# Optimization experiments

Hardware: AMD Instinct MI355X
Metric: run time of the kernel (lower is better)

The kernel has to match this reference:

```python
import jax, jax.numpy as jnp
import numpy as np

B, N, E, D = 1024, 6, 6, 1280  # batch, n_node, n_edge_types, state_dim
N_STEPS = 5
EDGES = [[1, 1, 2], [1, 2, 3], [1, 3, 4], [2, 4, 3], [2, 5, 4], [3, 6, 4]]


def make_adjacency():
    a = np.zeros([N, N * E * 2], dtype=np.float32)
    for src, et, tgt in EDGES:
        a[tgt - 1, (et - 1) * N + src - 1] = 1.0
        a[src - 1, (et - 1 + E) * N + tgt - 1] = 1.0
    return jnp.asarray(a)


def setup_inputs() -> dict:
    key = jax.random.key(0)
    ks = jax.random.split(key, 8)
    std = 0.02  # matches m.weight.data.normal_(0.0, 0.02)
    return {
        "x": jax.random.normal(ks[0], (B, N, D), jnp.float32),
        "A": make_adjacency(),  # [N, 2*E*N] structural 0/1 adjacency
        "W_in": std * jax.random.normal(ks[1], (E, D, D), jnp.float32),
        "b_in": jnp.zeros((E, D), jnp.float32),
        "W_out": std * jax.random.normal(ks[2], (E, D, D), jnp.float32),
        "b_out": jnp.zeros((E, D), jnp.float32),
        "W_r": std * jax.random.normal(ks[3], (3 * D, D), jnp.float32),
        "b_r": jnp.zeros((D,), jnp.float32),
        "W_z": std * jax.random.normal(ks[4], (3 * D, D), jnp.float32),
        "b_z": jnp.zeros((D,), jnp.float32),
        "W_t": std * jax.random.normal(ks[5], (3 * D, D), jnp.float32),
        "b_t": jnp.zeros((D,), jnp.float32),
    }


def reference(x, A, W_in, b_in, W_out, b_out, W_r, b_r, W_z, b_z, W_t, b_t):
    # x: [B, N, D] pooled per-part features (post backbone avgpool+transpose).
    A_in = A[:, : N * E]   # [N, E*N]
    A_out = A[:, N * E:]   # [N, E*N]
    gx = x
    for _ in range(N_STEPS):
        # per-edge-type linears; edge-type-major layout matches torch view(-1, N*E, D)
        in_s = jnp.einsum("bnd,edf->benf", gx, W_in) + b_in[:, None, :]   # [B,E,N,D]
        out_s = jnp.einsum("bnd,edf->benf", gx, W_out) + b_out[:, None, :]
        in_s = in_s.reshape(gx.shape[0], E * N, D)
        out_s = out_s.reshape(gx.shape[0], E * N, D)
        a_in = jnp.einsum("nm,bmd->bnd", A_in, in_s)     # bmm with adjacency
        a_out = jnp.einsum("nm,bmd->bnd", A_out, out_s)
        a = jnp.concatenate([a_in, a_out, gx], axis=-1)  # [B,N,3D]
        r = jax.nn.sigmoid(a @ W_r + b_r)
        z = jax.nn.sigmoid(a @ W_z + b_z)
        joined = jnp.concatenate([a_in, a_out, r * gx], axis=-1)
        h_hat = jnp.tanh(joined @ W_t + b_t)
        gx = (1.0 - z) * gx + z * h_hat
    # transpose(1,2) then flatten(1): [B, D, N] -> [B, D*N]
    return jnp.transpose(gx, (0, 2, 1)).reshape(gx.shape[0], D * N)
```

## Files before the change

kernel.cpp:

```cpp
#include <hip/hip_runtime.h>
#include <hip/hip_bf16.h>
#include <stdint.h>

#define D 1280
#define ND 6
#define BATCH 1024
#define ROWSTRIDE (ND*D)
#define WELEM (D*D)
#define WIOF(e) ((e)*WELEM)
#define WOOF(e) ((6+(e))*WELEM)
#define WROF (12*WELEM)
#define WZOF (15*WELEM)
#define WTOF (18*WELEM)
#define WTOT (21*WELEM)
#define ABUF (BATCH*ROWSTRIDE)
#define AINO (ABUF)
#define AOUTO (2*ABUF)
#define RGO (3*ABUF)
#define S3D (3*D)

typedef unsigned int u32;
typedef unsigned short u16;
typedef __bf16 bf16x8 __attribute__((ext_vector_type(8)));
typedef float f32x4 __attribute__((ext_vector_type(4)));

struct Term { int a_off; int b_off; int b_stride; int bias_off; };
struct Job  { int nterms; int epi; int node; int flag; Term t[3]; };

__constant__ Job JOBS[28] = {
  {1,0,1,0, {{0*D, WIOF(0), D, 0*D},{0,0,0,0},{0,0,0,0}}},
  {2,0,2,0, {{0*D, WIOF(1), D, 1*D},{1*D, WIOF(3), D, 3*D},{0,0,0,0}}},
  {3,0,3,0, {{0*D, WIOF(2), D, 2*D},{1*D, WIOF(4), D, 4*D},{2*D, WIOF(5), D, 5*D}}},
  {3,0,0,1, {{1*D, WOOF(0), D, 0*D},{2*D, WOOF(1), D, 1*D},{3*D, WOOF(2), D, 2*D}}},
  {2,0,1,1, {{2*D, WOOF(3), D, 3*D},{3*D, WOOF(4), D, 4*D},{0,0,0,0}}},
  {1,0,2,1, {{3*D, WOOF(5), D, 5*D},{0,0,0,0},{0,0,0,0}}},
  {2,1,0,0, {{AOUTO+0*D, WROF+1*D, S3D, 0},{0*D, WROF+2*D, S3D, 0},{0,0,0,0}}},
  {3,1,1,0, {{AINO+1*D, WROF+0*D, S3D, 0},{AOUTO+1*D, WROF+1*D, S3D, 0},{1*D, WROF+2*D, S3D, 0}}},
  {3,1,2,0, {{AINO+2*D, WROF+0*D, S3D, 0},{AOUTO+2*D, WROF+1*D, S3D, 0},{2*D, WROF+2*D, S3D, 0}}},
  {2,1,3,0, {{AINO+3*D, WROF+0*D, S3D, 0},{3*D, WROF+2*D, S3D, 0},{0,0,0,0}}},
  {1,1,4,0, {{4*D, WROF+2*D, S3D, 0},{0,0,0,0},{0,0,0,0}}},
  {1,1,5,0, {{5*D, WROF+2*D, S3D, 0},{0,0,0,0},{0,0,0,0}}},
  {2,2,0,0, {{AOUTO+0*D, WZOF+1*D, S3D, 0},{0*D, WZOF+2*D, S3D, 0},{0,0,0,0}}},
  {3,2,1,0, {{AINO+1*D, WZOF+0*D, S3D, 0},{AOUTO+1*D, WZOF+1*D, S3D, 0},{1*D, WZOF+2*D, S3D, 0}}},
  {3,2,2,0, {{AINO+2*D, WZOF+0*D, S3D, 0},{AOUTO+2*D, WZOF+1*D, S3D, 0},{2*D, WZOF+2*D, S3D, 0}}},
  {2,2,3,0, {{AINO+3*D, WZOF+0*D, S3D, 0},{3*D, WZOF+2*D, S3D, 0},{0,0,0,0}}},
  {1,2,4,0, {{4*D, WZOF+2*D, S3D, 0},{0,0,0,0},{0,0,0,0}}},
  {1,2,5,0, {{5*D, WZOF+2*D, S3D, 0},{0,0,0,0},{0,0,0,0}}},
  {1,3,0,0, {{AOUTO+0*D, WTOF+1*D, S3D, 0},{0,0,0,0},{0,0,0,0}}},
  {2,3,1,0, {{AINO+1*D, WTOF+0*D, S3D, 0},{AOUTO+1*D, WTOF+1*D, S3D, 0},{0,0,0,0}}},
  {2,3,2,0, {{AINO+2*D, WTOF+0*D, S3D, 0},{AOUTO+2*D, WTOF+1*D, S3D, 0},{0,0,0,0}}},
  {1,3,3,0, {{AINO+3*D, WTOF+0*D, S3D, 0},{0,0,0,0},{0,0,0,0}}},
  {1,4,0,1, {{RGO+0*D, WTOF+2*D, S3D, 0},{0,0,0,0},{0,0,0,0}}},
  {1,4,1,1, {{RGO+1*D, WTOF+2*D, S3D, 0},{0,0,0,0},{0,0,0,0}}},
  {1,4,2,1, {{RGO+2*D, WTOF+2*D, S3D, 0},{0,0,0,0},{0,0,0,0}}},
  {1,4,3,1, {{RGO+3*D, WTOF+2*D, S3D, 0},{0,0,0,0},{0,0,0,0}}},
  {1,4,4,0, {{RGO+4*D, WTOF+2*D, S3D, 0},{0,0,0,0},{0,0,0,0}}},
  {1,4,5,0, {{RGO+5*D, WTOF+2*D, S3D, 0},{0,0,0,0},{0,0,0,0}}},
};

__device__ __forceinline__ void gload16(const void* g, void* l) {
  __builtin_amdgcn_global_load_lds((const __attribute__((address_space(1))) u32*)g,
                                   (__attribute__((address_space(3))) u32*)l, 16, 0, 0);
}
__device__ __forceinline__ float sig_(float x){ return 1.f/(1.f+__expf(-x)); }
__device__ __forceinline__ float tanh_(float x){ float e=__expf(2.f*x); return 1.f-2.f/(e+1.f); }

__device__ __forceinline__ u16 f2b(float f){ __hip_bfloat16 v = __float2bfloat16(f); return *(u16*)&v; }

__global__ __launch_bounds__(256)
void gemm_batched(u16* act, const u16* __restrict__ wb,
                  float* __restrict__ gx, float* __restrict__ zbuf, float* __restrict__ tp,
                  const float* __restrict__ b_in, const float* __restrict__ b_out,
                  const float* __restrict__ b_r, const float* __restrict__ b_z,
                  const float* __restrict__ b_t, int job_base) {
  const int bid = blockIdx.x;
  const Job jb = JOBS[job_base + bid/80];
  const int t80 = bid % 80;
  const int m0 = (t80/10)*128;
  const int n0 = (t80%10)*128;
  const int tid = threadIdx.x;
  const int lane = tid & 63;
  const int w = tid >> 6;
  const int wm = ((w>>1)<<6);
  const int wn = ((w&1)<<6);

  __shared__ __align__(16) u16 lsA[128*64];
  __shared__ __align__(16) u16 lsB[128*64];

  f32x4 acc[4][4];
#pragma unroll
  for (int i=0;i<4;i++)
#pragma unroll
    for (int j=0;j<4;j++) acc[i][j] = (f32x4)(0.0f);

  const int srow = lane>>3;
  const int scol = (lane&7)*8;

  for (int term=0; term<jb.nterms; ++term) {
    const u16* Ab = act + jb.t[term].a_off;
    const u16* Bb = wb  + jb.t[term].b_off;
    const int bstr = jb.t[term].b_stride;
    for (int kt=0; kt<20; ++kt) {
      const int kk = kt*64;
#pragma unroll
      for (int i=0;i<4;i++) {
        const int rr = w*32 + i*8 + srow;
        gload16(Ab + (size_t)(m0+rr)*ROWSTRIDE + kk + scol, &lsA[(w*32+i*8)*64]);
        gload16(Bb + (size_t)(n0+rr)*bstr      + kk + scol, &lsB[(w*32+i*8)*64]);
      }
      __syncthreads();
#pragma unroll
      for (int ks=0; ks<2; ++ks) {
        bf16x8 af[4], bfr[4];
#pragma unroll
        for (int i=0;i<4;i++) {
          af[i]  = *(const bf16x8*)&lsA[(wm + i*16 + (lane&15))*64 + ks*32 + (lane>>4)*8];
          bfr[i] = *(const bf16x8*)&lsB[(wn + i*16 + (lane&15))*64 + ks*32 + (lane>>4)*8];
        }
#pragma unroll
        for (int i=0;i<4;i++)
#pragma unroll
          for (int j=0;j<4;j++)
            acc[i][j] = __builtin_amdgcn_mfma_f32_16x16x32_bf16(af[i], bfr[j], acc[i][j], 0,0,0);
      }
      __syncthreads();
    }
  }

  const int r0 = m0 + wm + ((lane>>4)<<2);
  const int c0 = n0 + wn + (lane&15);
  const int node = jb.node;

  if (jb.epi == 0) {
    const float* bias = jb.flag ? b_out : b_in;
    u16* outp = act + (jb.flag ? AOUTO : AINO) + node*D;
    float bsum[4];
#pragma unroll
    for (int j=0;j<4;j++) {
      float s = 0.f;
      for (int t2=0;t2<jb.nterms;t2++) s += bias[jb.t[t2].bias_off + c0 + j*16];
      bsum[j] = s;
    }
#pragma unroll
    for (int i=0;i<4;i++)
#pragma unroll
      for (int j=0;j<4;j++)
#pragma unroll
        for (int r=0;r<4;r++) {
          int row = r0 + i*16 + r, col = c0 + j*16;
          outp[(size_t)row*ROWSTRIDE + col] = f2b(acc[i][j][r] + bsum[j]);
        }
  } else if (jb.epi == 1) {
#pragma unroll
    for (int i=0;i<4;i++)
#pragma unroll
      for (int j=0;j<4;j++)
#pragma unroll
        for (int r=0;r<4;r++) {
          int row = r0 + i*16 + r, col = c0 + j*16;
          size_t idx = (size_t)row*ROWSTRIDE + node*D + col;
          float rr = sig_(acc[i][j][r] + b_r[col]);
          act[RGO + idx] = f2b(rr * gx[idx]);
        }
  } else if (jb.epi == 2) {
#pragma unroll
    for (int i=0;i<4;i++)
#pragma unroll
      for (int j=0;j<4;j++)
#pragma unroll
        for (int r=0;r<4;r++) {
          int row = r0 + i*16 + r, col = c0 + j*16;
          size_t idx = (size_t)row*ROWSTRIDE + node*D + col;
          zbuf[idx] = sig_(acc[i][j][r] + b_z[col]);
        }
  } else if (jb.epi == 3) {
#pragma unroll
    for (int i=0;i<4;i++)
#pragma unroll
      for (int j=0;j<4;j++)
#pragma unroll
        for (int r=0;r<4;r++) {
          int row = r0 + i*16 + r, col = c0 + j*16;
          size_t idx = (size_t)row*ROWSTRIDE + node*D + col;
          tp[idx] = acc[i][j][r];
        }
  } else {
#pragma unroll
    for (int i=0;i<4;i++)
#pragma unroll
      for (int j=0;j<4;j++)
#pragma unroll
        for (int r=0;r<4;r++) {
          int row = r0 + i*16 + r, col = c0 + j*16;
          size_t idx = (size_t)row*ROWSTRIDE + node*D + col;
          float tv = acc[i][j][r] + b_t[col] + (jb.flag ? tp[idx] : 0.f);
          float h = tanh_(tv);
          float zv = zbuf[idx];
          float g = gx[idx];
          float ng = (1.f - zv)*g + zv*h;
          gx[idx] = ng;
          act[idx] = f2b(ng);
        }
  }
}

__global__ void conv_weights(const float* __restrict__ wi, const float* __restrict__ wo,
                             const float* __restrict__ wr, const float* __restrict__ wz,
                             const float* __restrict__ wt, u16* __restrict__ wb) {
  int bid = blockIdx.x;
  int base = 0; int j = 0;
  for (; j < 15; ++j) {
    int R_ = (j < 12) ? 1280 : 3840;
    int tiles = (R_/32)*40;
    if (bid < base + tiles) break;
    base += tiles;
  }
  const int R = (j < 12) ? 1280 : 3840;
  const int C = 1280;
  const float* src; int doff;
  if (j < 6)        { src = wi + (size_t)j*WELEM;     doff = WIOF(j); }
  else if (j < 12)  { src = wo + (size_t)(j-6)*WELEM; doff = WOOF(j-6); }
  else if (j == 12) { src = wr;                       doff = WROF; }
  else if (j == 13) { src = wz;                       doff = WZOF; }
  else              { src = wt;                       doff = WTOF; }
  int tt = bid - base;
  int tr = tt / 40, tc = tt % 40;
  __shared__ float tile[32][33];
  int tx = threadIdx.x, ty = threadIdx.y;
#pragma unroll
  for (int k=0;k<4;k++)
    tile[ty+8*k][tx] = src[(size_t)(tr*32+ty+8*k)*C + tc*32+tx];
  __syncthreads();
  u16* dst = wb + doff;
#pragma unroll
  for (int k=0;k<4;k++)
    dst[(size_t)(tc*32+ty+8*k)*R + tr*32+tx] = f2b(tile[tx][ty+8*k]);
}

__global__ void init_gx(const float* __restrict__ x, float* __restrict__ gx, u16* __restrict__ gxb) {
  for (size_t i = (size_t)blockIdx.x*blockDim.x + threadIdx.x; i < (size_t)ABUF;
       i += (size_t)gridDim.x*blockDim.x) {
    float v = x[i];
    gx[i] = v;
    gxb[i] = f2b(v);
  }
}

__global__ void final_out(const float* __restrict__ gx, float* __restrict__ out) {
  int b = blockIdx.x;
  const float* g = gx + (size_t)b*ROWSTRIDE;
  float* o = out + (size_t)b*ROWSTRIDE;
  for (int jj = threadIdx.x; jj < ROWSTRIDE; jj += blockDim.x) {
    int n = jj % ND, d = jj / ND;
    o[jj] = g[n*D + d];
  }
}

extern "C" void kernel_launch(void* const* d_in, const int* in_sizes, int n_in,
                              void* d_out, int out_size, void* d_ws, size_t ws_size,
                              hipStream_t stream) {
  (void)in_sizes; (void)n_in; (void)out_size; (void)ws_size;
  const float* x  = (const float*)d_in[0];
  const float* Wi = (const float*)d_in[2];
  const float* bi = (const float*)d_in[3];
  const float* Wo = (const float*)d_in[4];
  const float* bo = (const float*)d_in[5];
  const float* Wr = (const float*)d_in[6];
  const float* br = (const float*)d_in[7];
  const float* Wz = (const float*)d_in[8];
  const float* bz = (const float*)d_in[9];
  const float* Wt = (const float*)d_in[10];
  const float* bt = (const float*)d_in[11];
  float* out = (float*)d_out;

  u16* wb  = (u16*)d_ws;
  u16* act = wb + WTOT;
  float* gx = (float*)(act + (size_t)4*ABUF);
  float* zb = gx + ABUF;
  float* tp = zb + ABUF;

  conv_weights<<<33600, dim3(32,8,1), 0, stream>>>(Wi, Wo, Wr, Wz, Wt, wb);
  init_gx<<<2048, 256, 0, stream>>>(x, gx, act);
  for (int s = 0; s < 5; ++s) {
    gemm_batched<<<480, 256, 0, stream>>>(act, wb, gx, zb, tp, bi, bo, br, bz, bt, 0);
    gemm_batched<<<1280,256, 0, stream>>>(act, wb, gx, zb, tp, bi, bo, br, bz, bt, 6);
    gemm_batched<<<480, 256, 0, stream>>>(act, wb, gx, zb, tp, bi, bo, br, bz, bt, 22);
  }
  final_out<<<BATCH, 256, 0, stream>>>(gx, out);
}
```

Measured before the change: 1.909 ms.

## Rewrite GEMM with 256x256 tiles, LDS double buffering, and split edge-term combine

Replaces the 128x128 single-buffered GEMM with a 512-thread, 256x256-tile kernel. It double-buffers LDS through async global-to-LDS loads, uses an XOR-swizzled LDS layout, raises instruction priority around the MFMA blocks, and interleaves loads of the next tile with compute in four phases. The multi-term edge GEMMs are split into 12 single-term jobs whose bf16 partial results land in a scratch buffer. A new combine kernel then sums those partials, which adds an extra launch and an extra round trip to memory. The gate jobs are reordered so the heavier ones are scheduled first.

```diff
diff --git a/kernel.cpp b/kernel.cpp
--- a/kernel.cpp
+++ b/kernel.cpp
@@ -18,37 +18,45 @@
 #define AOUTO (2*ABUF)
 #define RGO (3*ABUF)
 #define S3D (3*D)
+#define SLICE (BATCH*D)
 
 typedef unsigned int u32;
 typedef unsigned short u16;
 typedef __bf16 bf16x8 __attribute__((ext_vector_type(8)));
 typedef float f32x4 __attribute__((ext_vector_type(4)));
+typedef u16 u16x8 __attribute__((ext_vector_type(8)));
 
 struct Term { int a_off; int b_off; int b_stride; int bias_off; };
 struct Job  { int nterms; int epi; int node; int flag; Term t[3]; };
 
-__constant__ Job JOBS[28] = {
-  {1,0,1,0, {{0*D, WIOF(0), D, 0*D},{0,0,0,0},{0,0,0,0}}},
-  {2,0,2,0, {{0*D, WIOF(1), D, 1*D},{1*D, WIOF(3), D, 3*D},{0,0,0,0}}},
-  {3,0,3,0, {{0*D, WIOF(2), D, 2*D},{1*D, WIOF(4), D, 4*D},{2*D, WIOF(5), D, 5*D}}},
-  {3,0,0,1, {{1*D, WOOF(0), D, 0*D},{2*D, WOOF(1), D, 1*D},{3*D, WOOF(2), D, 2*D}}},
-  {2,0,1,1, {{2*D, WOOF(3), D, 3*D},{3*D, WOOF(4), D, 4*D},{0,0,0,0}}},
-  {1,0,2,1, {{3*D, WOOF(5), D, 5*D},{0,0,0,0},{0,0,0,0}}},
-  {2,1,0,0, {{AOUTO+0*D, WROF+1*D, S3D, 0},{0*D, WROF+2*D, S3D, 0},{0,0,0,0}}},
+__constant__ Job JOBS[34] = {
+  {1,0,0, 0, {{0*D, WIOF(0), D, 0*D},{0,0,0,0},{0,0,0,0}}},
+  {1,0,1, 0, {{0*D, WIOF(1), D, 1*D},{0,0,0,0},{0,0,0,0}}},
+  {1,0,2, 0, {{0*D, WIOF(2), D, 2*D},{0,0,0,0},{0,0,0,0}}},
+  {1,0,3, 0, {{1*D, WIOF(3), D, 3*D},{0,0,0,0},{0,0,0,0}}},
+  {1,0,4, 0, {{1*D, WIOF(4), D, 4*D},{0,0,0,0},{0,0,0,0}}},
+  {1,0,5, 0, {{2*D, WIOF(5), D, 5*D},{0,0,0,0},{0,0,0,0}}},
+  {1,0,6, 1, {{1*D, WOOF(0), D, 0*D},{0,0,0,0},{0,0,0,0}}},
+  {1,0,7, 1, {{2*D, WOOF(1), D, 1*D},{0,0,0,0},{0,0,0,0}}},
+  {1,0,8, 1, {{3*D, WOOF(2), D, 2*D},{0,0,0,0},{0,0,0,0}}},
+  {1,0,9, 1, {{2*D, WOOF(3), D, 3*D},{0,0,0,0},{0,0,0,0}}},
+  {1,0,10,1, {{3*D, WOOF(4), D, 4*D},{0,0,0,0},{0,0,0,0}}},
+  {1,0,11,1, {{3*D, WOOF(5), D, 5*D},{0,0,0,0},{0,0,0,0}}},
   {3,1,1,0, {{AINO+1*D, WROF+0*D, S3D, 0},{AOUTO+1*D, WROF+1*D, S3D, 0},{1*D, WROF+2*D, S3D, 0}}},
   {3,1,2,0, {{AINO+2*D, WROF+0*D, S3D, 0},{AOUTO+2*D, WROF+1*D, S3D, 0},{2*D, WROF+2*D, S3D, 0}}},
+  {3,2,1,0, {{AINO+1*D, WZOF+0*D, S3D, 0},{AOUTO+1*D, WZOF+1*D, S3D, 0},{1*D, WZOF+2*D, S3D, 0}}},
+  {3,2,2,0, {{AINO+2*D, WZOF+0*D, S3D, 0},{AOUTO+2*D, WZOF+1*D, S3D, 0},{2*D, WZOF+2*D, S3D, 0}}},
+  {2,1,0,0, {{AOUTO+0*D, WROF+1*D, S3D, 0},{0*D, WROF+2*D, S3D, 0},{0,0,0,0}}},
   {2,1,3,0, {{AINO+3*D, WROF+0*D, S3D, 0},{3*D, WROF+2*D, S3D, 0},{0,0,0,0}}},
+  {2,2,0,0, {{AOUTO+0*D, WZOF+1*D, S3D, 0},{0*D, WZOF+2*D, S3D, 0},{0,0,0,0}}},
+  {2,2,3,0, {{AINO+3*D, WZOF+0*D, S3D, 0},{3*D, WZOF+2*D, S3D, 0},{0,0,0,0}}},
+  {2,3,1,0, {{AINO+1*D, WTOF+0*D, S3D, 0},{AOUTO+1*D, WTOF+1*D, S3D, 0},{0,0,0,0}}},
+  {2,3,2,0, {{AINO+2*D, WTOF+0*D, S3D, 0},{AOUTO+2*D, WTOF+1*D, S3D, 0},{0,0,0,0}}},
   {1,1,4,0, {{4*D, WROF+2*D, S3D, 0},{0,0,0,0},{0,0,0,0}}},
   {1,1,5,0, {{5*D, WROF+2*D, S3D, 0},{0,0,0,0},{0,0,0,0}}},
-  {2,2,0,0, {{AOUTO+0*D, WZOF+1*D, S3D, 0},{0*D, WZOF+2*D, S3D, 0},{0,0,0,0}}},
-  {3,2,1,0, {{AINO+1*D, WZOF+0*D, S3D, 0},{AOUTO+1*D, WZOF+1*D, S3D, 0},{1*D, WZOF+2*D, S3D, 0}}},
-  {3,2,2,0, {{AINO+2*D, WZOF+0*D, S3D, 0},{AOUTO+2*D, WZOF+1*D, S3D, 0},{2*D, WZOF+2*D, S3D, 0}}},
-  {2,2,3,0, {{AINO+3*D, WZOF+0*D, S3D, 0},{3*D, WZOF+2*D, S3D, 0},{0,0,0,0}}},
   {1,2,4,0, {{4*D, WZOF+2*D, S3D, 0},{0,0,0,0},{0,0,0,0}}},
   {1,2,5,0, {{5*D, WZOF+2*D, S3D, 0},{0,0,0,0},{0,0,0,0}}},
   {1,3,0,0, {{AOUTO+0*D, WTOF+1*D, S3D, 0},{0,0,0,0},{0,0,0,0}}},
-  {2,3,1,0, {{AINO+1*D, WTOF+0*D, S3D, 0},{AOUTO+1*D, WTOF+1*D, S3D, 0},{0,0,0,0}}},
-  {2,3,2,0, {{AINO+2*D, WTOF+0*D, S3D, 0},{AOUTO+2*D, WTOF+1*D, S3D, 0},{0,0,0,0}}},
   {1,3,3,0, {{AINO+3*D, WTOF+0*D, S3D, 0},{0,0,0,0},{0,0,0,0}}},
   {1,4,0,1, {{RGO+0*D, WTOF+2*D, S3D, 0},{0,0,0,0},{0,0,0,0}}},
   {1,4,1,1, {{RGO+1*D, WTOF+2*D, S3D, 0},{0,0,0,0},{0,0,0,0}}},
@@ -58,150 +66,282 @@
   {1,4,5,0, {{RGO+5*D, WTOF+2*D, S3D, 0},{0,0,0,0},{0,0,0,0}}},
 };
 
+struct Cmb { int dst; int np; int p[3]; };
+__constant__ Cmb CMBS[6] = {
+  {AINO + 1*D, 1, {0,0,0}},
+  {AINO + 2*D, 2, {1,3,0}},
+  {AINO + 3*D, 3, {2,4,5}},
+  {AOUTO+ 0*D, 3, {6,7,8}},
+  {AOUTO+ 1*D, 2, {9,10,0}},
+  {AOUTO+ 2*D, 1, {11,0,0}},
+};
+
 __device__ __forceinline__ void gload16(const void* g, void* l) {
   __builtin_amdgcn_global_load_lds((const __attribute__((address_space(1))) u32*)g,
                                    (__attribute__((address_space(3))) u32*)l, 16, 0, 0);
 }
 __device__ __forceinline__ float sig_(float x){ return 1.f/(1.f+__expf(-x)); }
 __device__ __forceinline__ float tanh_(float x){ float e=__expf(2.f*x); return 1.f-2.f/(e+1.f); }
-
 __device__ __forceinline__ u16 f2b(float f){ __hip_bfloat16 v = __float2bfloat16(f); return *(u16*)&v; }
-
-__global__ __launch_bounds__(256)
-void gemm_batched(u16* act, const u16* __restrict__ wb,
-                  float* __restrict__ gx, float* __restrict__ zbuf, float* __restrict__ tp,
-                  const float* __restrict__ b_in, const float* __restrict__ b_out,
-                  const float* __restrict__ b_r, const float* __restrict__ b_z,
-                  const float* __restrict__ b_t, int job_base) {
-  const int bid = blockIdx.x;
-  const Job jb = JOBS[job_base + bid/80];
-  const int t80 = bid % 80;
-  const int m0 = (t80/10)*128;
-  const int n0 = (t80%10)*128;
-  const int tid = threadIdx.x;
+__device__ __forceinline__ float b2f(u16 v){ return __uint_as_float(((u32)v)<<16); }
+
+__device__ __forceinline__ void bar() {
+  asm volatile("" ::: "memory");
+  __builtin_amdgcn_s_barrier();
+  asm volatile("" ::: "memory");
+}
+#define VMCNT(n) asm volatile("s_waitcnt vmcnt(" #n ")" ::: "memory")
+
+__device__ __forceinline__ void stage_part(int jidx, const u16* __restrict__ act,
+    const u16* __restrict__ wb, u16* ls, int m0, int n0, int Ts, int part,
+    int lane, int w) {
+  const int tm = (Ts >= 40) ? 2 : (Ts >= 20 ? 1 : 0);
+  const int kt = Ts - tm*20;
+  const Term& t = JOBS[jidx].t[tm];
+  const u16* G; int gstr; int row0;
+  if (part < 2) { G = act + t.a_off; gstr = ROWSTRIDE;  row0 = m0 + part*128; }
+  else          { G = wb  + t.b_off; gstr = t.b_stride; row0 = n0 + (part-2)*128; }
+  u16* lbase = ls + (part < 2 ? 0 : 32768) + (((Ts&1)*2 + (part&1))*8192);
+  const u16* gk = G + kt*64;
+#pragma unroll
+  for (int l = 0; l < 2; ++l) {
+    const int rb = l*64 + w*8;
+    const int r  = rb + (lane>>3);
+    const int c  = ((lane&7)*8) ^ ((r&4) ? 16 : 0);
+    gload16(gk + (size_t)(row0 + r)*gstr + c, lbase + rb*64);
+  }
+}
+
+__global__ __launch_bounds__(512, 1)
+void gemm256(u16* __restrict__ act, const u16* __restrict__ wb, u16* __restrict__ part,
+             float* __restrict__ gx, float* __restrict__ zbuf, float* __restrict__ tp,
+             const float* __restrict__ b_in, const float* __restrict__ b_out,
+             const float* __restrict__ b_r, const float* __restrict__ b_z,
+             const float* __restrict__ b_t, int job_base) {
+  extern __shared__ u16 ls[];
+  const int bid  = blockIdx.x;
+  const int jidx = job_base + bid/20;
+  const int tile = bid%20;
+  const int m0 = (tile/5)*256;
+  const int n0 = (tile%5)*256;
+  const int tid  = threadIdx.x;
   const int lane = tid & 63;
-  const int w = tid >> 6;
-  const int wm = ((w>>1)<<6);
-  const int wn = ((w&1)<<6);
-
-  __shared__ __align__(16) u16 lsA[128*64];
-  __shared__ __align__(16) u16 lsB[128*64];
-
-  f32x4 acc[4][4];
-#pragma unroll
-  for (int i=0;i<4;i++)
-#pragma unroll
-    for (int j=0;j<4;j++) acc[i][j] = (f32x4)(0.0f);
-
-  const int srow = lane>>3;
-  const int scol = (lane&7)*8;
-
-  for (int term=0; term<jb.nterms; ++term) {
-    const u16* Ab = act + jb.t[term].a_off;
-    const u16* Bb = wb  + jb.t[term].b_off;
-    const int bstr = jb.t[term].b_stride;
-    for (int kt=0; kt<20; ++kt) {
-      const int kk = kt*64;
-#pragma unroll
-      for (int i=0;i<4;i++) {
-        const int rr = w*32 + i*8 + srow;
-        gload16(Ab + (size_t)(m0+rr)*ROWSTRIDE + kk + scol, &lsA[(w*32+i*8)*64]);
-        gload16(Bb + (size_t)(n0+rr)*bstr      + kk + scol, &lsB[(w*32+i*8)*64]);
+  const int w    = tid >> 6;
+  const int wm   = w >> 2;
+  const int wn   = w & 3;
+  const int NT   = JOBS[jidx].nterms * 20;
+
+  f32x4 acc[8][4];
+#pragma unroll
+  for (int f=0; f<8; ++f)
+#pragma unroll
+    for (int g=0; g<4; ++g) acc[f][g] = (f32x4)(0.0f);
+
+  stage_part(jidx, act, wb, ls, m0, n0, 0, 0, lane, w);
+  stage_part(jidx, act, wb, ls, m0, n0, 0, 1, lane, w);
+  stage_part(jidx, act, wb, ls, m0, n0, 0, 2, lane, w);
+  stage_part(jidx, act, wb, ls, m0, n0, 0, 3, lane, w);
+  stage_part(jidx, act, wb, ls, m0, n0, 1, 2, lane, w);
+  stage_part(jidx, act, wb, ls, m0, n0, 1, 3, lane, w);
+  VMCNT(4);
+  bar();
+
+  const int lr = lane & 15;
+  const int lc = (lane >> 4) * 8;
+
+  for (int T = 0; T < NT; ++T) {
+    const int d = T & 1;
+    const u16* Ah = ls + (d*2 + wm)*8192;
+    const u16* Bh = ls + 32768 + (d*2 + (wn>>1))*8192;
+    bf16x8 af[4][2], b01[2][2], b23[2][2];
+
+#pragma unroll
+    for (int fi=0; fi<4; ++fi)
+#pragma unroll
+      for (int ks=0; ks<2; ++ks) {
+        const int r = fi*16 + lr;
+        const int c = (ks*32 + lc) ^ ((r&4) ? 16 : 0);
+        af[fi][ks] = *(const bf16x8*)(Ah + r*64 + c);
       }
-      __syncthreads();
+#pragma unroll
+    for (int g=0; g<2; ++g)
 #pragma unroll
       for (int ks=0; ks<2; ++ks) {
-        bf16x8 af[4], bfr[4];
-#pragma unroll
-        for (int i=0;i<4;i++) {
-          af[i]  = *(const bf16x8*)&lsA[(wm + i*16 + (lane&15))*64 + ks*32 + (lane>>4)*8];
-          bfr[i] = *(const bf16x8*)&lsB[(wn + i*16 + (lane&15))*64 + ks*32 + (lane>>4)*8];
+        const int r = (wn&1)*64 + g*16 + lr;
+        const int c = (ks*32 + lc) ^ ((r&4) ? 16 : 0);
+        b01[g][ks] = *(const bf16x8*)(Bh + r*64 + c);
+      }
+    if (T+1 < NT) stage_part(jidx, act, wb, ls, m0, n0, T+1, 0, lane, w);
+    bar();
+    __builtin_amdgcn_s_setprio(1);
+#pragma unroll
+    for (int fi=0; fi<4; ++fi)
+#pragma unroll
+      for (int g=0; g<2; ++g)
+#pragma unroll
+        for (int ks=0; ks<2; ++ks)
+          acc[fi][g] = __builtin_amdgcn_mfma_f32_16x16x32_bf16(af[fi][ks], b01[g][ks], acc[fi][g], 0,0,0);
+    __builtin_amdgcn_s_setprio(0);
+    bar();
+
+#pragma unroll
+    for (int g=0; g<2; ++g)
+#pragma unroll
+      for (int ks=0; ks<2; ++ks) {
+        const int r = (wn&1)*64 + (g+2)*16 + lr;
+        const int c = (ks*32 + lc) ^ ((r&4) ? 16 : 0);
+        b23[g][ks] = *(const bf16x8*)(Bh + r*64 + c);
+      }
+    if (T+1 < NT) stage_part(jidx, act, wb, ls, m0, n0, T+1, 1, lane, w);
+    bar();
+    __builtin_amdgcn_s_setprio(1);
+#pragma unroll
+    for (int fi=0; fi<4; ++fi)
+#pragma unroll
+      for (int g=0; g<2; ++g)
+#pragma unroll
+        for (int ks=0; ks<2; ++ks)
+          acc[fi][g+2] = __builtin_amdgcn_mfma_f32_16x16x32_bf16(af[fi][ks], b23[g][ks], acc[fi][g+2], 0,0,0);
+    __builtin_amdgcn_s_setprio(0);
+    bar();
+
+#pragma unroll
+    for (int fi=0; fi<4; ++fi)
+#pragma unroll
+      for (int ks=0; ks<2; ++ks) {
+        const int r = (fi+4)*16 + lr;
+        const int c = (ks*32 + lc) ^ ((r&4) ? 16 : 0);
+        af[fi][ks] = *(const bf16x8*)(Ah + r*64 + c);
+      }
+    if (T+2 < NT) stage_part(jidx, act, wb, ls, m0, n0, T+2, 2, lane, w);
+    bar();
+    __builtin_amdgcn_s_setprio(1);
+#pragma unroll
+    for (int fi=0; fi<4; ++fi)
+#pragma unroll
+      for (int g=0; g<2; ++g)
+#pragma unroll
+        for (int ks=0; ks<2; ++ks)
+          acc[fi+4][g] = __builtin_amdgcn_mfma_f32_16x16x32_bf16(af[fi][ks], b01[g][ks], acc[fi+4][g], 0,0,0);
+    __builtin_amdgcn_s_setprio(0);
+    bar();
+
+    if (T+2 < NT) {
+      stage_part(jidx, act, wb, ls, m0, n0, T+2, 3, lane, w);
+      VMCNT(4);
+    } else {
+      VMCNT(0);
+    }
+    bar();
+    __builtin_amdgcn_s_setprio(1);
+#pragma unroll
+    for (int fi=0; fi<4; ++fi)
+#pragma unroll
+      for (int g=0; g<2; ++g)
+#pragma unroll
+        for (int ks=0; ks<2; ++ks)
+          acc[fi+4][g+2] = __builtin_amdgcn_mfma_f32_16x16x32_bf16(af[fi][ks], b23[g][ks], acc[fi+4][g+2], 0,0,0);
+    __builtin_amdgcn_s_setprio(0);
+    bar();
+  }
+
+  const int epi  = JOBS[jidx].epi;
+  const int node = JOBS[jidx].node;
+  const int flag = JOBS[jidx].flag;
+  const int r0 = m0 + wm*128 + ((lane>>4)<<2);
+  const int c0 = n0 + wn*64 + (lane&15);
+
+  if (epi == 0) {
+    const float* bias = (flag ? b_out : b_in) + JOBS[jidx].t[0].bias_off;
+    u16* outp = part + (size_t)node*SLICE;
+#pragma unroll
+    for (int g=0; g<4; ++g) {
+      const int col = c0 + g*16;
+      const float bv = bias[col];
+#pragma unroll
+      for (int f=0; f<8; ++f)
+#pragma unroll
+        for (int r=0; r<4; ++r)
+          outp[(size_t)(r0 + f*16 + r)*D + col] = f2b(acc[f][g][r] + bv);
+    }
+  } else if (epi == 1) {
+#pragma unroll
+    for (int g=0; g<4; ++g) {
+      const int col = c0 + g*16;
+      const float bv = b_r[col];
+#pragma unroll
+      for (int f=0; f<8; ++f)
+#pragma unroll
+        for (int r=0; r<4; ++r) {
+          const size_t idx = (size_t)(r0 + f*16 + r)*ROWSTRIDE + node*D + col;
+          act[RGO + idx] = f2b(sig_(acc[f][g][r] + bv) * gx[idx]);
         }
-#pragma unroll
-        for (int i=0;i<4;i++)
-#pragma unroll
-          for (int j=0;j<4;j++)
-            acc[i][j] = __builtin_amdgcn_mfma_f32_16x16x32_bf16(af[i], bfr[j], acc[i][j], 0,0,0);
-      }
-      __syncthreads();
-    }
-  }
-
-  const int r0 = m0 + wm + ((lane>>4)<<2);
-  const int c0 = n0 + wn + (lane&15);
-  const int node = jb.node;
-
-  if (jb.epi == 0) {
-    const float* bias = jb.flag ? b_out : b_in;
-    u16* outp = act + (jb.flag ? AOUTO : AINO) + node*D;
-    float bsum[4];
-#pragma unroll
-    for (int j=0;j<4;j++) {
-      float s = 0.f;
-      for (int t2=0;t2<jb.nterms;t2++) s += bias[jb.t[t2].bias_off + c0 + j*16];
-      bsum[j] = s;
-    }
-#pragma unroll
-    for (int i=0;i<4;i++)
-#pragma unroll
-      for (int j=0;j<4;j++)
-#pragma unroll
-        for (int r=0;r<4;r++) {
-          int row = r0 + i*16 + r, col = c0 + j*16;
-          outp[(size_t)row*ROWSTRIDE + col] = f2b(acc[i][j][r] + bsum[j]);
+    }
+  } else if (epi == 2) {
+#pragma unroll
+    for (int g=0; g<4; ++g) {
+      const int col = c0 + g*16;
+      const float bv = b_z[col];
+#pragma unroll
+      for (int f=0; f<8; ++f)
+#pragma unroll
+        for (int r=0; r<4; ++r) {
+          const size_t idx = (size_t)(r0 + f*16 + r)*ROWSTRIDE + node*D + col;
+          zbuf[idx] = sig_(acc[f][g][r] + bv);
         }
-  } else if (jb.epi == 1) {
-#pragma unroll
-    for (int i=0;i<4;i++)
-#pragma unroll
-      for (int j=0;j<4;j++)
-#pragma unroll
-        for (int r=0;r<4;r++) {
-          int row = r0 + i*16 + r, col = c0 + j*16;
-          size_t idx = (size_t)row*ROWSTRIDE + node*D + col;
-          float rr = sig_(acc[i][j][r] + b_r[col]);
-          act[RGO + idx] = f2b(rr * gx[idx]);
+    }
+  } else if (epi == 3) {
+#pragma unroll
+    for (int g=0; g<4; ++g) {
+      const int col = c0 + g*16;
+#pragma unroll
+      for (int f=0; f<8; ++f)
+#pragma unroll
+        for (int r=0; r<4; ++r) {
+          const size_t idx = (size_t)(r0 + f*16 + r)*ROWSTRIDE + node*D + col;
+          tp[idx] = acc[f][g][r];
         }
-  } else if (jb.epi == 2) {
-#pragma unroll
-    for (int i=0;i<4;i++)
-#pragma unroll
-      for (int j=0;j<4;j++)
-#pragma unroll
-        for (int r=0;r<4;r++) {
-          int row = r0 + i*16 + r, col = c0 + j*16;
-          size_t idx = (size_t)row*ROWSTRIDE + node*D + col;
-          zbuf[idx] = sig_(acc[i][j][r] + b_z[col]);
-        }
-  } else if (jb.epi == 3) {
-#pragma unroll
-    for (int i=0;i<4;i++)
-#pragma unroll
-      for (int j=0;j<4;j++)
-#pragma unroll
-        for (int r=0;r<4;r++) {
-          int row = r0 + i*16 + r, col = c0 + j*16;
-          size_t idx = (size_t)row*ROWSTRIDE + node*D + col;
-          tp[idx] = acc[i][j][r];
-        }
+    }
   } else {
 #pragma unroll
-    for (int i=0;i<4;i++)
-#pragma unroll
-      for (int j=0;j<4;j++)
-#pragma unroll
-        for (int r=0;r<4;r++) {
-          int row = r0 + i*16 + r, col = c0 + j*16;
-          size_t idx = (size_t)row*ROWSTRIDE + node*D + col;
-          float tv = acc[i][j][r] + b_t[col] + (jb.flag ? tp[idx] : 0.f);
-          float h = tanh_(tv);
+    for (int g=0; g<4; ++g) {
+      const int col = c0 + g*16;
+      const float bv = b_t[col];
+#pragma unroll
+      for (int f=0; f<8; ++f)
+#pragma unroll
+        for (int r=0; r<4; ++r) {
+          const size_t idx = (size_t)(r0 + f*16 + r)*ROWSTRIDE + node*D + col;
+          float tv = acc[f][g][r] + bv + (flag ? tp[idx] : 0.f);
+          float h  = tanh_(tv);
           float zv = zbuf[idx];
-          float g = gx[idx];
-          float ng = (1.f - zv)*g + zv*h;
-          gx[idx] = ng;
+          float gv = gx[idx];
+          float ng = (1.f - zv)*gv + zv*h;
+          gx[idx]  = ng;
           act[idx] = f2b(ng);
         }
-  }
+    }
+  }
+}
+
+__global__ void combine(u16* __restrict__ act, const u16* __restrict__ part) {
+  const int bid = blockIdx.x;
+  const int s = bid/640;
+  const int idx = (bid%640)*256 + threadIdx.x;
+  const int row = idx/160, c8 = (idx%160)*8;
+  const Cmb& cb = CMBS[s];
+  float sum[8];
+#pragma unroll
+  for (int q=0;q<8;q++) sum[q]=0.f;
+  for (int i=0;i<cb.np;i++) {
+    const u16x8 v = *(const u16x8*)(part + (size_t)cb.p[i]*SLICE + (size_t)row*D + c8);
+#pragma unroll
+    for (int q=0;q<8;q++) sum[q] += b2f(v[q]);
+  }
+  u16x8 o;
+#pragma unroll
+  for (int q=0;q<8;q++) o[q] = f2b(sum[q]);
+  *(u16x8*)(act + (size_t)cb.dst + (size_t)row*ROWSTRIDE + c8) = o;
 }
 
 __global__ void conv_weights(const float* __restrict__ wi, const float* __restrict__ wo,
@@ -275,16 +415,18 @@
 
   u16* wb  = (u16*)d_ws;
   u16* act = wb + WTOT;
-  float* gx = (float*)(act + (size_t)4*ABUF);
-  float* zb = gx + ABUF;
-  float* tp = zb + ABUF;
+  float* gxp = (float*)(act + (size_t)4*ABUF);
+  float* zb  = gxp + ABUF;
+  float* tpp = zb + ABUF;
+  u16* partp = (u16*)tpp;
 
   conv_weights<<<33600, dim3(32,8,1), 0, stream>>>(Wi, Wo, Wr, Wz, Wt, wb);
-  init_gx<<<2048, 256, 0, stream>>>(x, gx, act);
+  init_gx<<<2048, 256, 0, stream>>>(x, gxp, act);
   for (int s = 0; s < 5; ++s) {
-    gemm_batched<<<480, 256, 0, stream>>>(act, wb, gx, zb, tp, bi, bo, br, bz, bt, 0);
-    gemm_batched<<<1280,256, 0, stream>>>(act, wb, gx, zb, tp, bi, bo, br, bz, bt, 6);
-    gemm_batched<<<480, 256, 0, stream>>>(act, wb, gx, zb, tp, bi, bo, br, bz, bt, 22);
-  }
-  final_out<<<BATCH, 256, 0, stream>>>(gx, out);
-}
+    gemm256<<<240, 512, 131072, stream>>>(act, wb, partp, gxp, zb, tpp, bi, bo, br, bz, bt, 0);
+    combine<<<3840, 256, 0, stream>>>(act, partp);
+    gemm256<<<320, 512, 131072, stream>>>(act, wb, partp, gxp, zb, tpp, bi, bo, br, bz, bt, 12);
+    gemm256<<<120, 512, 131072, stream>>>(act, wb, partp, gxp, zb, tpp, bi, bo, br, bz, bt, 28);
+  }
+  final_out<<<BATCH, 256, 0, stream>>>(gxp, out);
+}
```

Result: slower. 2.353 ms (+23.2%).

## Double-buffer LDS tiles with XOR swizzle, flatten term loop, remap blocks to XCDs

Applied to the files above, without the earlier changes.

The GEMM main loop now uses two LDS buffers and prefetches the next K-tile, including across term boundaries, while MFMAs run on the current tile. Each iteration then needs one barrier instead of two. LDS columns are XOR-swizzled to cut bank conflicts on the fragment reads. Block IDs are remapped so consecutive work lands on the same XCD, and the job table is reordered so heavy 3-term jobs are interleaved with light ones for load balance. In exchange the kernel uses twice the LDS (64KB) with a launch bound of 2 blocks per CU, and the job order and block mapping it assumes are more intricate.

```diff
diff --git a/kernel.cpp b/kernel.cpp
--- a/kernel.cpp
+++ b/kernel.cpp
@@ -28,26 +28,26 @@
 struct Job  { int nterms; int epi; int node; int flag; Term t[3]; };
 
 __constant__ Job JOBS[28] = {
+  {3,0,3,0, {{0*D, WIOF(2), D, 2*D},{1*D, WIOF(4), D, 4*D},{2*D, WIOF(5), D, 5*D}}},
   {1,0,1,0, {{0*D, WIOF(0), D, 0*D},{0,0,0,0},{0,0,0,0}}},
   {2,0,2,0, {{0*D, WIOF(1), D, 1*D},{1*D, WIOF(3), D, 3*D},{0,0,0,0}}},
-  {3,0,3,0, {{0*D, WIOF(2), D, 2*D},{1*D, WIOF(4), D, 4*D},{2*D, WIOF(5), D, 5*D}}},
   {3,0,0,1, {{1*D, WOOF(0), D, 0*D},{2*D, WOOF(1), D, 1*D},{3*D, WOOF(2), D, 2*D}}},
+  {1,0,2,1, {{3*D, WOOF(5), D, 5*D},{0,0,0,0},{0,0,0,0}}},
   {2,0,1,1, {{2*D, WOOF(3), D, 3*D},{3*D, WOOF(4), D, 4*D},{0,0,0,0}}},
-  {1,0,2,1, {{3*D, WOOF(5), D, 5*D},{0,0,0,0},{0,0,0,0}}},
+  {3,1,1,0, {{AINO+1*D, WROF+0*D, S3D, 0},{AOUTO+1*D, WROF+1*D, S3D, 0},{1*D, WROF+2*D, S3D, 0}}},
+  {1,1,4,0, {{4*D, WROF+2*D, S3D, 0},{0,0,0,0},{0,0,0,0}}},
+  {3,1,2,0, {{AINO+2*D, WROF+0*D, S3D, 0},{AOUTO+2*D, WROF+1*D, S3D, 0},{2*D, WROF+2*D, S3D, 0}}},
+  {1,1,5,0, {{5*D, WROF+2*D, S3D, 0},{0,0,0,0},{0,0,0,0}}},
+  {3,2,1,0, {{AINO+1*D, WZOF+0*D, S3D, 0},{AOUTO+1*D, WZOF+1*D, S3D, 0},{1*D, WZOF+2*D, S3D, 0}}},
+  {1,2,4,0, {{4*D, WZOF+2*D, S3D, 0},{0,0,0,0},{0,0,0,0}}},
+  {3,2,2,0, {{AINO+2*D, WZOF+0*D, S3D, 0},{AOUTO+2*D, WZOF+1*D, S3D, 0},{2*D, WZOF+2*D, S3D, 0}}},
+  {1,2,5,0, {{5*D, WZOF+2*D, S3D, 0},{0,0,0,0},{0,0,0,0}}},
   {2,1,0,0, {{AOUTO+0*D, WROF+1*D, S3D, 0},{0*D, WROF+2*D, S3D, 0},{0,0,0,0}}},
-  {3,1,1,0, {{AINO+1*D, WROF+0*D, S3D, 0},{AOUTO+1*D, WROF+1*D, S3D, 0},{1*D, WROF+2*D, S3D, 0}}},
-  {3,1,2,0, {{AINO+2*D, WROF+0*D, S3D, 0},{AOUTO+2*D, WROF+1*D, S3D, 0},{2*D, WROF+2*D, S3D, 0}}},
   {2,1,3,0, {{AINO+3*D, WROF+0*D, S3D, 0},{3*D, WROF+2*D, S3D, 0},{0,0,0,0}}},
-  {1,1,4,0, {{4*D, WROF+2*D, S3D, 0},{0,0,0,0},{0,0,0,0}}},
-  {1,1,5,0, {{5*D, WROF+2*D, S3D, 0},{0,0,0,0},{0,0,0,0}}},
   {2,2,0,0, {{AOUTO+0*D, WZOF+1*D, S3D, 0},{0*D, WZOF+2*D, S3D, 0},{0,0,0,0}}},
-  {3,2,1,0, {{AINO+1*D, WZOF+0*D, S3D, 0},{AOUTO+1*D, WZOF+1*D, S3D, 0},{1*D, WZOF+2*D, S3D, 0}}},
-  {3,2,2,0, {{AINO+2*D, WZOF+0*D, S3D, 0},{AOUTO+2*D, WZOF+1*D, S3D, 0},{2*D, WZOF+2*D, S3D, 0}}},
   {2,2,3,0, {{AINO+3*D, WZOF+0*D, S3D, 0},{3*D, WZOF+2*D, S3D, 0},{0,0,0,0}}},
-  {1,2,4,0, {{4*D, WZOF+2*D, S3D, 0},{0,0,0,0},{0,0,0,0}}},
-  {1,2,5,0, {{5*D, WZOF+2*D, S3D, 0},{0,0,0,0},{0,0,0,0}}},
+  {2,3,1,0, {{AINO+1*D, WTOF+0*D, S3D, 0},{AOUTO+1*D, WTOF+1*D, S3D, 0},{0,0,0,0}}},
   {1,3,0,0, {{AOUTO+0*D, WTOF+1*D, S3D, 0},{0,0,0,0},{0,0,0,0}}},
-  {2,3,1,0, {{AINO+1*D, WTOF+0*D, S3D, 0},{AOUTO+1*D, WTOF+1*D, S3D, 0},{0,0,0,0}}},
   {2,3,2,0, {{AINO+2*D, WTOF+0*D, S3D, 0},{AOUTO+2*D, WTOF+1*D, S3D, 0},{0,0,0,0}}},
   {1,3,3,0, {{AINO+3*D, WTOF+0*D, S3D, 0},{0,0,0,0},{0,0,0,0}}},
   {1,4,0,1, {{RGO+0*D, WTOF+2*D, S3D, 0},{0,0,0,0},{0,0,0,0}}},
@@ -64,28 +64,51 @@
 }
 __device__ __forceinline__ float sig_(float x){ return 1.f/(1.f+__expf(-x)); }
 __device__ __forceinline__ float tanh_(float x){ float e=__expf(2.f*x); return 1.f-2.f/(e+1.f); }
-
 __device__ __forceinline__ u16 f2b(float f){ __hip_bfloat16 v = __float2bfloat16(f); return *(u16*)&v; }
 
-__global__ __launch_bounds__(256)
-void gemm_batched(u16* act, const u16* __restrict__ wb,
+__device__ __forceinline__ void stageAB(const u16* __restrict__ A, const u16* __restrict__ Bb,
+    int bstr, u16* la, u16* lb, int kk, int tid) {
+  const int rr = tid >> 3;
+  const int ce = (tid & 7) * 8;
+  const int wbase = (tid >> 6) * 512;
+#pragma unroll
+  for (int c4 = 0; c4 < 4; ++c4) {
+    const int r  = c4*32 + rr;
+    const int cs = ce ^ ((r & 7) << 3);
+    gload16(A  + (size_t)r*ROWSTRIDE + (size_t)kk + cs, la + c4*2048 + wbase);
+    gload16(Bb + (size_t)r*bstr      + (size_t)kk + cs, lb + c4*2048 + wbase);
+  }
+}
+
+__global__ __launch_bounds__(256, 2)
+void gemm_batched(u16* __restrict__ act, const u16* __restrict__ wb,
                   float* __restrict__ gx, float* __restrict__ zbuf, float* __restrict__ tp,
                   const float* __restrict__ b_in, const float* __restrict__ b_out,
                   const float* __restrict__ b_r, const float* __restrict__ b_z,
                   const float* __restrict__ b_t, int job_base) {
-  const int bid = blockIdx.x;
-  const Job jb = JOBS[job_base + bid/80];
-  const int t80 = bid % 80;
-  const int m0 = (t80/10)*128;
-  const int n0 = (t80%10)*128;
-  const int tid = threadIdx.x;
+  __shared__ __align__(16) u16 lsA[2][128*64];
+  __shared__ __align__(16) u16 lsB[2][128*64];
+  const int cpx = gridDim.x >> 3;
+  const int wid = (blockIdx.x & 7)*cpx + (blockIdx.x >> 3);
+  const int job = wid / 80;
+  const int rem = wid % 80;
+  const int n0 = (rem >> 3) * 128;
+  const int m0 = (rem & 7) * 128;
+  const int tid  = threadIdx.x;
   const int lane = tid & 63;
-  const int w = tid >> 6;
-  const int wm = ((w>>1)<<6);
-  const int wn = ((w&1)<<6);
-
-  __shared__ __align__(16) u16 lsA[128*64];
-  __shared__ __align__(16) u16 lsB[128*64];
+  const int w    = tid >> 6;
+  const int wm   = (w >> 1) << 6;
+  const int wn   = (w & 1) << 6;
+  const Job jb = JOBS[job_base + job];
+  const int NT = jb.nterms * 20;
+
+  const u16* At[3]; const u16* Bt[3]; int bs[3];
+#pragma unroll
+  for (int i=0;i<3;i++) {
+    At[i] = act + jb.t[i].a_off + (size_t)m0*ROWSTRIDE;
+    Bt[i] = wb  + jb.t[i].b_off + (size_t)n0*jb.t[i].b_stride;
+    bs[i] = jb.t[i].b_stride;
+  }
 
   f32x4 acc[4][4];
 #pragma unroll
@@ -93,42 +116,43 @@
 #pragma unroll
     for (int j=0;j<4;j++) acc[i][j] = (f32x4)(0.0f);
 
-  const int srow = lane>>3;
-  const int scol = (lane&7)*8;
-
-  for (int term=0; term<jb.nterms; ++term) {
-    const u16* Ab = act + jb.t[term].a_off;
-    const u16* Bb = wb  + jb.t[term].b_off;
-    const int bstr = jb.t[term].b_stride;
-    for (int kt=0; kt<20; ++kt) {
-      const int kk = kt*64;
+  stageAB(At[0], Bt[0], bs[0], lsA[0], lsB[0], 0, tid);
+  __syncthreads();
+
+  const int lr = lane & 15;
+  const int lc = (lane >> 4) * 8;
+
+  for (int t = 0; t < NT; ++t) {
+    if (t+1 < NT) {
+      const int tm = (t+1)/20;
+      const int kk = ((t+1)%20)*64;
+      stageAB(At[tm], Bt[tm], bs[tm], lsA[(t+1)&1], lsB[(t+1)&1], kk, tid);
+    }
+    const u16* la = lsA[t&1];
+    const u16* lb = lsB[t&1];
+#pragma unroll
+    for (int ks=0; ks<2; ++ks) {
+      bf16x8 af[4], bfr[4];
 #pragma unroll
       for (int i=0;i<4;i++) {
-        const int rr = w*32 + i*8 + srow;
-        gload16(Ab + (size_t)(m0+rr)*ROWSTRIDE + kk + scol, &lsA[(w*32+i*8)*64]);
-        gload16(Bb + (size_t)(n0+rr)*bstr      + kk + scol, &lsB[(w*32+i*8)*64]);
+        const int ra = wm + i*16 + lr;
+        const int ca = (ks*32 + lc) ^ ((ra&7)<<3);
+        af[i]  = *(const bf16x8*)(la + ra*64 + ca);
+        const int rb = wn + i*16 + lr;
+        const int cb = (ks*32 + lc) ^ ((rb&7)<<3);
+        bfr[i] = *(const bf16x8*)(lb + rb*64 + cb);
       }
-      __syncthreads();
-#pragma unroll
-      for (int ks=0; ks<2; ++ks) {
-        bf16x8 af[4], bfr[4];
-#pragma unroll
-        for (int i=0;i<4;i++) {
-          af[i]  = *(const bf16x8*)&lsA[(wm + i*16 + (lane&15))*64 + ks*32 + (lane>>4)*8];
-          bfr[i] = *(const bf16x8*)&lsB[(wn + i*16 + (lane&15))*64 + ks*32 + (lane>>4)*8];
-        }
-#pragma unroll
-        for (int i=0;i<4;i++)
-#pragma unroll
-          for (int j=0;j<4;j++)
-            acc[i][j] = __builtin_amdgcn_mfma_f32_16x16x32_bf16(af[i], bfr[j], acc[i][j], 0,0,0);
-      }
-      __syncthreads();
+#pragma unroll
+      for (int i=0;i<4;i++)
+#pragma unroll
+        for (int j=0;j<4;j++)
+          acc[i][j] = __builtin_amdgcn_mfma_f32_16x16x32_bf16(af[i], bfr[j], acc[i][j], 0,0,0);
     }
+    __syncthreads();
   }
 
   const int r0 = m0 + wm + ((lane>>4)<<2);
-  const int c0 = n0 + wn + (lane&15);
+  const int c0 = n0 + wn + lr;
   const int node = jb.node;
 
   if (jb.epi == 0) {
@@ -275,16 +299,16 @@
 
   u16* wb  = (u16*)d_ws;
   u16* act = wb + WTOT;
-  float* gx = (float*)(act + (size_t)4*ABUF);
-  float* zb = gx + ABUF;
-  float* tp = zb + ABUF;
+  float* gxp = (float*)(act + (size_t)4*ABUF);
+  float* zb  = gxp + ABUF;
+  float* tpp = zb + ABUF;
 
   conv_weights<<<33600, dim3(32,8,1), 0, stream>>>(Wi, Wo, Wr, Wz, Wt, wb);
-  init_gx<<<2048, 256, 0, stream>>>(x, gx, act);
+  init_gx<<<2048, 256, 0, stream>>>(x, gxp, act);
   for (int s = 0; s < 5; ++s) {
-    gemm_batched<<<480, 256, 0, stream>>>(act, wb, gx, zb, tp, bi, bo, br, bz, bt, 0);
-    gemm_batched<<<1280,256, 0, stream>>>(act, wb, gx, zb, tp, bi, bo, br, bz, bt, 6);
-    gemm_batched<<<480, 256, 0, stream>>>(act, wb, gx, zb, tp, bi, bo, br, bz, bt, 22);
-  }
-  final_out<<<BATCH, 256, 0, stream>>>(gx, out);
-}
+    gemm_batched<<<480, 256, 0, stream>>>(act, wb, gxp, zb, tpp, bi, bo, br, bz, bt, 0);
+    gemm_batched<<<1280,256, 0, stream>>>(act, wb, gxp, zb, tpp, bi, bo, br, bz, bt, 6);
+    gemm_batched<<<480, 256, 0, stream>>>(act, wb, gxp, zb, tpp, bi, bo, br, bz, bt, 22);
+  }
+  final_out<<<BATCH, 256, 0, stream>>>(gxp, out);
+}
```

Measured after the change: 1.962 ms. 2.7% more time.
